# Optimization experiments

Measured on AMD Instinct MI355X. Metric: run time of the kernel, lower is better.

The kernel has to match this reference:

```python
import jax, jax.numpy as jnp
import numpy as np

EPS = 1e-5  # norm_eps


def setup_inputs() -> dict:
    key = jax.random.key(0)
    ks = jax.random.split(key, 9)
    N, C, T, H, W = 2, 1024, 8, 28, 28
    Di = 512
    s = 0.02  # weight init scale
    return {
        "x": jax.random.normal(ks[0], (N, C, T, H, W), jnp.float32),
        "w_theta": jax.random.normal(ks[1], (Di, C), jnp.float32) * s,
        "b_theta": jax.random.normal(ks[2], (Di,), jnp.float32) * s,
        "w_phi": jax.random.normal(ks[3], (Di, C), jnp.float32) * s,
        "b_phi": jax.random.normal(ks[4], (Di,), jnp.float32) * s,
        "w_g": jax.random.normal(ks[5], (Di, C), jnp.float32) * s,
        "b_g": jax.random.normal(ks[6], (Di,), jnp.float32) * s,
        "w_out": jax.random.normal(ks[7], (C, Di), jnp.float32) * s,
        "b_out": jax.random.normal(ks[8], (C,), jnp.float32) * s,
    }


def reference(x, w_theta, b_theta, w_phi, b_phi, w_g, b_g, w_out, b_out):
    # ProgressNL forward at step==0 (y == x), pool_size=None,
    # instantiation='softmax', norm_type='layernorm' (GroupNorm(1, C, affine=False)).
    N, C, T, H, W = x.shape
    Di = w_theta.shape[0]
    xf = x.reshape(N, C, T * H * W)  # flatten spatio-temporal tokens

    # 1x1x1 convs == per-token matmuls
    theta = jnp.einsum('dc,nct->ndt', w_theta, xf) + b_theta[None, :, None]  # [N,Di,THW]
    phi = jnp.einsum('dc,nct->ndt', w_phi, xf) + b_phi[None, :, None]
    g = jnp.einsum('dc,nct->ndt', w_g, xf) + b_g[None, :, None]

    # attention: softmax(theta^T phi / sqrt(Di)) @ g^T
    scores = jnp.einsum('nct,ncp->ntp', theta, phi) * (Di ** -0.5)  # [N,THW,THW]
    attn = jax.nn.softmax(scores, axis=-1)
    o = jnp.einsum('ntp,ncp->nct', attn, g)  # [N,Di,THW]

    # output 1x1x1 conv
    p = jnp.einsum('cd,ndt->nct', w_out, o) + b_out[None, :, None]  # [N,C,THW]

    # GroupNorm(1, C, affine=False): normalize over (C,T,H,W) per sample
    mean = jnp.mean(p, axis=(1, 2), keepdims=True)
    var = jnp.var(p, axis=(1, 2), keepdims=True)
    p = (p - mean) * jax.lax.rsqrt(var + EPS)

    return x + p.reshape(N, C, T, H, W)
```

## Files before the change

kernel.cpp:

```cpp
#include <hip/hip_runtime.h>

typedef _Float16 f16x8 __attribute__((ext_vector_type(8)));
typedef _Float16 f16x4 __attribute__((ext_vector_type(4)));
typedef float    f32x4 __attribute__((ext_vector_type(4)));

#define THW 6272
#define CCH 1024
#define DI  512

__device__ __forceinline__ void gload16(const _Float16* g, _Float16* l)
{
    __builtin_amdgcn_global_load_lds(
        (const __attribute__((address_space(1))) void*)g,
        (__attribute__((address_space(3))) void*)l, 16, 0, 0);
}

template<typename OUT_T, int BM, bool BIAS_M, bool BIAS_N, bool EXPP, bool GNP>
__global__ __launch_bounds__(256, 3)
void gemm_nt(const _Float16* __restrict__ A, size_t lda, size_t sAn,
             const _Float16* __restrict__ Bt, size_t ldb, size_t sBn,
             OUT_T* __restrict__ C, size_t ldc, size_t sCn,
             int K, float alpha,
             const float* __restrict__ bias_m,
             const float* __restrict__ bias_n,
             float* __restrict__ psum,
             int rows_ps,
             int gx, int gy)
{
    constexpr int MF = BM / 32;
    __shared__ _Float16 As[BM * 64];
    __shared__ _Float16 Bs[128 * 64];
    __shared__ float rs[4], rs2[4];
    const int tid  = threadIdx.x;
    const int lane = tid & 63;
    const int wave = tid >> 6;
    const int wr = wave >> 1, wc = wave & 1;

    const int nwg = gridDim.x;
    const int q = nwg >> 3, rr = nwg & 7;
    const int xcd = blockIdx.x & 7, seq = blockIdx.x >> 3;
    const int wg = (xcd < rr ? xcd * (q + 1) : rr * (q + 1) + (xcd - rr) * q) + seq;
    const int zz  = wg / (gx * gy);
    const int rem = wg - zz * gx * gy;
    const int by  = rem / gx, bx = rem - by * gx;
    const int n   = zz & 1;
    const int ks  = zz >> 1;

    A  += (size_t)n * sAn + (size_t)ks * K + (size_t)by * BM * lda;
    Bt += (size_t)n * sBn + (size_t)ks * K + (size_t)bx * 128 * ldb;

    const int srow = lane >> 3, sk = (lane & 7) * 8;
    const _Float16* gA = A  + (size_t)(wave * (MF * 8) + srow) * lda + sk;
    const _Float16* gB = Bt + (size_t)(wave * 32 + srow) * ldb + sk;
    _Float16* lA = As + wave * (MF * 512) + lane * 8;
    _Float16* lB = Bs + wave * 2048 + lane * 8;

    const int r  = lane & 15;
    const int kg = lane >> 4;

    f32x4 acc[MF][4] = {};

    for (int kt = 0; kt < K; kt += 64) {
#pragma unroll
        for (int i = 0; i < MF; i++)
            gload16(gA + (size_t)(i * 8) * lda, lA + i * 512);
#pragma unroll
        for (int i = 0; i < 4; i++)
            gload16(gB + (size_t)(i * 8) * ldb, lB + i * 512);
        gA += 64; gB += 64;
        __syncthreads();
#pragma unroll
        for (int kk = 0; kk < 2; kk++) {
            f16x8 af[MF], bf[4];
#pragma unroll
            for (int mf = 0; mf < MF; mf++)
                af[mf] = *(const f16x8*)(As + (wr * (BM / 2) + mf * 16 + r) * 64 + kk * 32 + kg * 8);
#pragma unroll
            for (int nf = 0; nf < 4; nf++)
                bf[nf] = *(const f16x8*)(Bs + (wc * 64 + nf * 16 + r) * 64 + kk * 32 + kg * 8);
#pragma unroll
            for (int mf = 0; mf < MF; mf++)
#pragma unroll
                for (int nf = 0; nf < 4; nf++)
                    acc[mf][nf] = __builtin_amdgcn_mfma_f32_16x16x32_f16(
                        af[mf], bf[nf], acc[mf][nf], 0, 0, 0);
        }
        __syncthreads();
    }

    C += (size_t)zz * sCn;
    float gs = 0.f, gs2 = 0.f;
#pragma unroll
    for (int mf = 0; mf < MF; mf++) {
#pragma unroll
        for (int qi = 0; qi < 4; qi++) {
            size_t row = (size_t)by * BM + wr * (BM / 2) + mf * 16 + kg * 4 + qi;
            float bm = BIAS_M ? bias_m[row] : 0.f;
            float rsum = 0.f;
#pragma unroll
            for (int nf = 0; nf < 4; nf++) {
                size_t col = (size_t)bx * 128 + wc * 64 + nf * 16 + r;
                float val = acc[mf][nf][qi] * alpha + bm + (BIAS_N ? bias_n[col] : 0.f);
                if (EXPP) {
                    float e = __expf(val);
                    rsum += e;
                    C[row * ldc + col] = (OUT_T)e;
                } else {
                    C[row * ldc + col] = (OUT_T)val;
                }
                if (GNP) { gs += val; gs2 += val * val; }
            }
            if (EXPP) {
                rsum += __shfl_xor(rsum, 1);
                rsum += __shfl_xor(rsum, 2);
                rsum += __shfl_xor(rsum, 4);
                rsum += __shfl_xor(rsum, 8);
                if (r == 0)
                    psum[((size_t)n * rows_ps + row) * 98 + bx * 2 + wc] = rsum;
            }
        }
    }
    if (GNP) {
        for (int o = 32; o; o >>= 1) {
            gs  += __shfl_xor(gs, o);
            gs2 += __shfl_xor(gs2, o);
        }
        if (lane == 0) { rs[wave] = gs; rs2[wave] = gs2; }
        __syncthreads();
        if (tid == 0) {
            psum[(size_t)wg * 2]     = rs[0] + rs[1] + rs[2] + rs[3];
            psum[(size_t)wg * 2 + 1] = rs2[0] + rs2[1] + rs2[2] + rs2[3];
        }
    }
}

__global__ __launch_bounds__(256)
void rowsum_inv(const float* __restrict__ psum, float* __restrict__ inv, int nrows)
{
    int rI = blockIdx.x * 256 + threadIdx.x;
    if (rI < nrows) {
        const float* p = psum + (size_t)rI * 98;
        float s = 0.f;
#pragma unroll 7
        for (int i = 0; i < 98; i++) s += p[i];
        inv[rI] = 1.f / s;
    }
}

__global__ __launch_bounds__(256)
void combine_scale(const float* __restrict__ Op, const float* __restrict__ inv,
                   _Float16* __restrict__ Ot, int tr, int t0)
{
    const int total4 = tr * 256;
    int idx = blockIdx.x * 256 + threadIdx.x;
    if (idx >= total4) return;
    const int per_n4 = tr * 128;
    int n = idx / per_n4;
    int rem = idx - n * per_n4;
    int t = rem >> 7, d4 = rem & 127;
    const f32x4* p = (const f32x4*)Op;
    f32x4 a = p[(size_t)n * per_n4 + rem];
    f32x4 b = p[(size_t)(2 + n) * per_n4 + rem];
    float sc = inv[(size_t)n * tr + t];
    f16x4 o;
#pragma unroll
    for (int j = 0; j < 4; j++) o[j] = (_Float16)((a[j] + b[j]) * sc);
    *(f16x4*)(Ot + ((size_t)(n * THW + t0 + t) * DI + d4 * 4)) = o;
}

__global__ __launch_bounds__(256)
void pack_weights(const float* __restrict__ wt, const float* __restrict__ wp,
                  const float* __restrict__ wg, const float* __restrict__ wo,
                  const float* __restrict__ bt, const float* __restrict__ bp,
                  _Float16* __restrict__ Wtp, _Float16* __restrict__ Wg,
                  _Float16* __restrict__ Wo, float* __restrict__ btp)
{
    int i = blockIdx.x * 256 + threadIdx.x;
    if (i < 512 * 1024) {
        Wtp[i]              = (_Float16)wt[i];
        Wtp[i + 512 * 1024] = (_Float16)wp[i];
        Wg[i]               = (_Float16)wg[i];
        Wo[i]               = (_Float16)wo[i];
    }
    if (i < 512) { btp[i] = bt[i]; btp[i + 512] = bp[i]; }
}

__global__ __launch_bounds__(256)
void transpose_cast(const float* __restrict__ x, _Float16* __restrict__ xT)
{
    __shared__ float tile[32][33];
    const int n  = blockIdx.z;
    const int t0 = blockIdx.x * 32;
    const int c0 = blockIdx.y * 32;
    const int tx = threadIdx.x & 31, ty = threadIdx.x >> 5;
    const float* xp = x + ((size_t)n * CCH + c0) * THW + t0;
#pragma unroll
    for (int i = 0; i < 4; i++) {
        int c = ty + i * 8;
        tile[c][tx] = xp[(size_t)c * THW + tx];
    }
    __syncthreads();
    _Float16* op = xT + ((size_t)n * THW + t0) * CCH + c0;
#pragma unroll
    for (int i = 0; i < 4; i++) {
        int t = ty + i * 8;
        op[(size_t)t * CCH + tx] = (_Float16)tile[tx][t];
    }
}

__global__ __launch_bounds__(256)
void reduce_final(const float* __restrict__ partials, float* __restrict__ stats, int nblk)
{
    const int n = blockIdx.x;
    float s = 0.f, s2 = 0.f;
    for (int i = threadIdx.x; i < nblk; i += 256) {
        s  += partials[((size_t)n * nblk + i) * 2];
        s2 += partials[((size_t)n * nblk + i) * 2 + 1];
    }
    for (int o = 32; o; o >>= 1) { s += __shfl_xor(s, o); s2 += __shfl_xor(s2, o); }
    __shared__ float rs[4], rs2[4];
    if ((threadIdx.x & 63) == 0) { rs[threadIdx.x >> 6] = s; rs2[threadIdx.x >> 6] = s2; }
    __syncthreads();
    if (threadIdx.x == 0) {
        float S1 = rs[0] + rs[1] + rs[2] + rs[3];
        float S2 = rs2[0] + rs2[1] + rs2[2] + rs2[3];
        const float invc = 1.f / ((float)CCH * (float)THW);
        float mean = S1 * invc;
        float var  = S2 * invc - mean * mean;
        stats[n * 2]     = mean;
        stats[n * 2 + 1] = rsqrtf(var + 1e-5f);
    }
}

__global__ __launch_bounds__(256)
void final_residual(const float* __restrict__ x, float* __restrict__ pc_out,
                    const float* __restrict__ stats, size_t total4)
{
    const size_t per_n4 = (size_t)CCH * THW / 4;
    for (size_t i = (size_t)blockIdx.x * 256 + threadIdx.x; i < total4;
         i += (size_t)gridDim.x * 256) {
        int n = (int)(i / per_n4);
        float mean = stats[n * 2], rstd = stats[n * 2 + 1];
        f32x4 xv = ((const f32x4*)x)[i];
        f32x4 pv = ((f32x4*)pc_out)[i];
        f32x4 ov;
#pragma unroll
        for (int j = 0; j < 4; j++) ov[j] = xv[j] + (pv[j] - mean) * rstd;
        ((f32x4*)pc_out)[i] = ov;
    }
}

extern "C" void kernel_launch(void* const* d_in, const int* in_sizes, int n_in,
                              void* d_out, int out_size, void* d_ws, size_t ws_size,
                              hipStream_t stream)
{
    const float* x  = (const float*)d_in[0];
    const float* wt = (const float*)d_in[1];
    const float* bt = (const float*)d_in[2];
    const float* wp = (const float*)d_in[3];
    const float* bp = (const float*)d_in[4];
    const float* wg = (const float*)d_in[5];
    const float* bg = (const float*)d_in[6];
    const float* wo = (const float*)d_in[7];
    const float* bo = (const float*)d_in[8];
    float* out = (float*)d_out;

    char* ws = (char*)d_ws;
    size_t off = 0;
    auto alloc = [&](size_t b) -> void* {
        off = (off + 255) & ~(size_t)255;
        void* p = ws + off;
        off += b;
        return p;
    };

    _Float16* Wtp = (_Float16*)alloc((size_t)1024 * 1024 * 2);
    _Float16* Wg  = (_Float16*)alloc((size_t)512 * 1024 * 2);
    _Float16* Wo  = (_Float16*)alloc((size_t)1024 * 512 * 2);
    float*    btp = (float*)alloc(1024 * 4);
    _Float16* xT  = (_Float16*)alloc((size_t)2 * THW * CCH * 2);
    _Float16* tpg = (_Float16*)alloc((size_t)2 * THW * 1024 * 2);
    _Float16* g   = (_Float16*)alloc((size_t)2 * DI * THW * 2);
    _Float16* Ot  = (_Float16*)alloc((size_t)2 * THW * DI * 2);
    float*    gnp   = (float*)alloc((size_t)784 * 2 * 4);
    float*    stats = (float*)alloc(4 * 4);

    const size_t tile_bytes = (size_t)2 * 128 * (THW * 2 + 98 * 4 + 4);
    size_t avail = (ws_size > off + 256) ? ws_size - off - 256 : 0;
    int tiles_fit = (int)(avail / tile_bytes);
    if (tiles_fit < 1) tiles_fit = 1;
    if (tiles_fit > 49) tiles_fit = 49;
    int nch = (49 + tiles_fit - 1) / tiles_fit;
    int tpc = (49 + nch - 1) / nch;

    _Float16* S    = (_Float16*)alloc((size_t)2 * tpc * 128 * THW * 2);
    float*    psum = (float*)alloc((size_t)2 * tpc * 128 * 98 * 4);
    float*    inv  = (float*)alloc((size_t)2 * tpc * 128 * 4);
    float*    Opart = out;

    const size_t sXT = (size_t)THW * CCH;
    const size_t sG  = (size_t)DI * THW;

    pack_weights<<<2048, 256, 0, stream>>>(wt, wp, wg, wo, bt, bp, Wtp, Wg, Wo, btp);
    transpose_cast<<<dim3(THW / 32, CCH / 32, 2), 256, 0, stream>>>(x, xT);

    gemm_nt<_Float16, 128, false, true, false, false><<<8 * 49 * 2, 256, 0, stream>>>(
        xT, CCH, sXT, Wtp, CCH, 0, tpg, 1024, sXT, CCH, 1.f,
        nullptr, btp, nullptr, 0, 8, 49);

    gemm_nt<_Float16, 64, true, false, false, false><<<49 * 8 * 2, 256, 0, stream>>>(
        Wg, CCH, 0, xT, CCH, sXT, g, THW, sG, CCH, 1.f,
        bg, nullptr, nullptr, 0, 49, 8);

    const float scale = 0.044194173824159216f;
    for (int ch = 0; ch < nch; ch++) {
        int tile0 = ch * tpc;
        int tiles = (49 - tile0 < tpc) ? (49 - tile0) : tpc;
        size_t t0 = (size_t)tile0 * 128;
        int tchRows = tiles * 128;

        gemm_nt<_Float16, 128, false, false, true, false><<<49 * tiles * 2, 256, 0, stream>>>(
            tpg + t0 * 1024, 1024, sXT, tpg + 512, 1024, sXT,
            S, THW, (size_t)tchRows * THW, DI, scale,
            nullptr, nullptr, psum, tchRows, 49, tiles);

        rowsum_inv<<<(2 * tchRows + 255) / 256, 256, 0, stream>>>(psum, inv, 2 * tchRows);

        gemm_nt<float, 128, false, false, false, false><<<4 * tiles * 4, 256, 0, stream>>>(
            S, THW, (size_t)tchRows * THW, g, THW, sG,
            Opart, DI, (size_t)tchRows * DI, THW / 2, 1.f,
            nullptr, nullptr, nullptr, 0, 4, tiles);

        combine_scale<<<(tchRows * 256 + 255) / 256, 256, 0, stream>>>(
            Opart, inv, Ot, tchRows, (int)t0);
    }

    gemm_nt<float, 128, true, false, false, true><<<49 * 8 * 2, 256, 0, stream>>>(
        Wo, DI, 0, Ot, DI, sG, out, THW, (size_t)CCH * THW, DI, 1.f,
        bo, nullptr, gnp, 0, 49, 8);

    reduce_final<<<2, 256, 0, stream>>>(gnp, stats, 392);
    final_residual<<<2048, 256, 0, stream>>>(x, out, stats, (size_t)2 * CCH * THW / 4);
}
```

Measured before the change: 452.3 us.

## Split attention PV GEMM four ways over K with fp16 partials and fused row scaling

The attention-times-g GEMM now splits its K dimension into four slices of 1600 instead of two halves, with a ragged last slice, which doubles the workgroup count for more parallelism. The softmax row normalization moves into the GEMM epilogue, and the partial outputs are stored as fp16 instead of fp32. The combine kernel becomes a 4-way fp16 sum. This targets low occupancy in the PV GEMM and the traffic of the partial buffers, at the cost of fp16 rounding on partial sums and an extra partial read in the combine step.

```diff
diff --git a/kernel.cpp b/kernel.cpp
--- a/kernel.cpp
+++ b/kernel.cpp
@@ -15,15 +15,16 @@
         (__attribute__((address_space(3))) void*)l, 16, 0, 0);
 }
 
-template<typename OUT_T, int BM, bool BIAS_M, bool BIAS_N, bool EXPP, bool GNP>
+template<typename OUT_T, int BM, bool BIAS_M, bool BIAS_N, bool EXPP, bool GNP, bool RSC>
 __global__ __launch_bounds__(256, 3)
 void gemm_nt(const _Float16* __restrict__ A, size_t lda, size_t sAn,
              const _Float16* __restrict__ Bt, size_t ldb, size_t sBn,
              OUT_T* __restrict__ C, size_t ldc, size_t sCn,
-             int K, float alpha,
+             int K, int Kfull, float alpha,
              const float* __restrict__ bias_m,
              const float* __restrict__ bias_n,
              float* __restrict__ psum,
+             const float* __restrict__ row_scale,
              int rows_ps,
              int gx, int gy)
 {
@@ -46,8 +47,11 @@
     const int n   = zz & 1;
     const int ks  = zz >> 1;
 
-    A  += (size_t)n * sAn + (size_t)ks * K + (size_t)by * BM * lda;
-    Bt += (size_t)n * sBn + (size_t)ks * K + (size_t)bx * 128 * ldb;
+    const int koff = ks * K;
+    const int klen = (Kfull - koff < K) ? (Kfull - koff) : K;
+
+    A  += (size_t)n * sAn + (size_t)by * BM * lda + koff;
+    Bt += (size_t)n * sBn + (size_t)bx * 128 * ldb + koff;
 
     const int srow = lane >> 3, sk = (lane & 7) * 8;
     const _Float16* gA = A  + (size_t)(wave * (MF * 8) + srow) * lda + sk;
@@ -60,7 +64,7 @@
 
     f32x4 acc[MF][4] = {};
 
-    for (int kt = 0; kt < K; kt += 64) {
+    for (int kt = 0; kt < klen; kt += 64) {
 #pragma unroll
         for (int i = 0; i < MF; i++)
             gload16(gA + (size_t)(i * 8) * lda, lA + i * 512);
@@ -96,6 +100,7 @@
         for (int qi = 0; qi < 4; qi++) {
             size_t row = (size_t)by * BM + wr * (BM / 2) + mf * 16 + kg * 4 + qi;
             float bm = BIAS_M ? bias_m[row] : 0.f;
+            float sc = RSC ? row_scale[(size_t)n * rows_ps + row] : 1.f;
             float rsum = 0.f;
 #pragma unroll
             for (int nf = 0; nf < 4; nf++) {
@@ -106,7 +111,7 @@
                     rsum += e;
                     C[row * ldc + col] = (OUT_T)e;
                 } else {
-                    C[row * ldc + col] = (OUT_T)val;
+                    C[row * ldc + col] = (OUT_T)(RSC ? val * sc : val);
                 }
                 if (GNP) { gs += val; gs2 += val * val; }
             }
@@ -148,24 +153,27 @@
 }
 
 __global__ __launch_bounds__(256)
-void combine_scale(const float* __restrict__ Op, const float* __restrict__ inv,
-                   _Float16* __restrict__ Ot, int tr, int t0)
-{
-    const int total4 = tr * 256;
+void combine4(const _Float16* __restrict__ Op, _Float16* __restrict__ Ot,
+              int tr, int t0)
+{
+    const int per_n8 = tr * 64;
     int idx = blockIdx.x * 256 + threadIdx.x;
-    if (idx >= total4) return;
-    const int per_n4 = tr * 128;
-    int n = idx / per_n4;
-    int rem = idx - n * per_n4;
-    int t = rem >> 7, d4 = rem & 127;
-    const f32x4* p = (const f32x4*)Op;
-    f32x4 a = p[(size_t)n * per_n4 + rem];
-    f32x4 b = p[(size_t)(2 + n) * per_n4 + rem];
-    float sc = inv[(size_t)n * tr + t];
-    f16x4 o;
-#pragma unroll
-    for (int j = 0; j < 4; j++) o[j] = (_Float16)((a[j] + b[j]) * sc);
-    *(f16x4*)(Ot + ((size_t)(n * THW + t0 + t) * DI + d4 * 4)) = o;
+    if (idx >= 2 * per_n8) return;
+    int n = idx / per_n8;
+    int rem = idx - n * per_n8;
+    int t = rem >> 6, d8 = rem & 63;
+    const size_t slice = (size_t)tr * 512;
+    float o[8] = {};
+#pragma unroll
+    for (int ks = 0; ks < 4; ks++) {
+        f16x8 v = *(const f16x8*)(Op + (size_t)(ks * 2 + n) * slice + (size_t)rem * 8);
+#pragma unroll
+        for (int j = 0; j < 8; j++) o[j] += (float)v[j];
+    }
+    f16x8 w;
+#pragma unroll
+    for (int j = 0; j < 8; j++) w[j] = (_Float16)o[j];
+    *(f16x8*)(Ot + ((size_t)(n * THW + t0 + t) * DI + d8 * 8)) = w;
 }
 
 __global__ __launch_bounds__(256)
@@ -296,7 +304,7 @@
     _Float16* S    = (_Float16*)alloc((size_t)2 * tpc * 128 * THW * 2);
     float*    psum = (float*)alloc((size_t)2 * tpc * 128 * 98 * 4);
     float*    inv  = (float*)alloc((size_t)2 * tpc * 128 * 4);
-    float*    Opart = out;
+    _Float16* Opart = (_Float16*)out;
 
     const size_t sXT = (size_t)THW * CCH;
     const size_t sG  = (size_t)DI * THW;
@@ -304,13 +312,13 @@
     pack_weights<<<2048, 256, 0, stream>>>(wt, wp, wg, wo, bt, bp, Wtp, Wg, Wo, btp);
     transpose_cast<<<dim3(THW / 32, CCH / 32, 2), 256, 0, stream>>>(x, xT);
 
-    gemm_nt<_Float16, 128, false, true, false, false><<<8 * 49 * 2, 256, 0, stream>>>(
-        xT, CCH, sXT, Wtp, CCH, 0, tpg, 1024, sXT, CCH, 1.f,
-        nullptr, btp, nullptr, 0, 8, 49);
-
-    gemm_nt<_Float16, 64, true, false, false, false><<<49 * 8 * 2, 256, 0, stream>>>(
-        Wg, CCH, 0, xT, CCH, sXT, g, THW, sG, CCH, 1.f,
-        bg, nullptr, nullptr, 0, 49, 8);
+    gemm_nt<_Float16, 128, false, true, false, false, false><<<8 * 49 * 2, 256, 0, stream>>>(
+        xT, CCH, sXT, Wtp, CCH, 0, tpg, 1024, sXT, CCH, CCH, 1.f,
+        nullptr, btp, nullptr, nullptr, 0, 8, 49);
+
+    gemm_nt<_Float16, 64, true, false, false, false, false><<<49 * 8 * 2, 256, 0, stream>>>(
+        Wg, CCH, 0, xT, CCH, sXT, g, THW, sG, CCH, CCH, 1.f,
+        bg, nullptr, nullptr, nullptr, 0, 49, 8);
 
     const float scale = 0.044194173824159216f;
     for (int ch = 0; ch < nch; ch++) {
@@ -319,25 +327,25 @@
         size_t t0 = (size_t)tile0 * 128;
         int tchRows = tiles * 128;
 
-        gemm_nt<_Float16, 128, false, false, true, false><<<49 * tiles * 2, 256, 0, stream>>>(
+        gemm_nt<_Float16, 128, false, false, true, false, false><<<49 * tiles * 2, 256, 0, stream>>>(
             tpg + t0 * 1024, 1024, sXT, tpg + 512, 1024, sXT,
-            S, THW, (size_t)tchRows * THW, DI, scale,
-            nullptr, nullptr, psum, tchRows, 49, tiles);
+            S, THW, (size_t)tchRows * THW, DI, DI, scale,
+            nullptr, nullptr, psum, nullptr, tchRows, 49, tiles);
 
         rowsum_inv<<<(2 * tchRows + 255) / 256, 256, 0, stream>>>(psum, inv, 2 * tchRows);
 
-        gemm_nt<float, 128, false, false, false, false><<<4 * tiles * 4, 256, 0, stream>>>(
+        gemm_nt<_Float16, 128, false, false, false, false, true><<<4 * tiles * 8, 256, 0, stream>>>(
             S, THW, (size_t)tchRows * THW, g, THW, sG,
-            Opart, DI, (size_t)tchRows * DI, THW / 2, 1.f,
-            nullptr, nullptr, nullptr, 0, 4, tiles);
-
-        combine_scale<<<(tchRows * 256 + 255) / 256, 256, 0, stream>>>(
-            Opart, inv, Ot, tchRows, (int)t0);
-    }
-
-    gemm_nt<float, 128, true, false, false, true><<<49 * 8 * 2, 256, 0, stream>>>(
-        Wo, DI, 0, Ot, DI, sG, out, THW, (size_t)CCH * THW, DI, 1.f,
-        bo, nullptr, gnp, 0, 49, 8);
+            Opart, DI, (size_t)tchRows * DI, 1600, THW, 1.f,
+            nullptr, nullptr, nullptr, inv, tchRows, 4, tiles);
+
+        combine4<<<(tchRows * 128 + 255) / 256, 256, 0, stream>>>(
+            Opart, Ot, tchRows, (int)t0);
+    }
+
+    gemm_nt<float, 128, true, false, false, true, false><<<49 * 8 * 2, 256, 0, stream>>>(
+        Wo, DI, 0, Ot, DI, sG, out, THW, (size_t)CCH * THW, DI, DI, 1.f,
+        bo, nullptr, gnp, nullptr, 0, 49, 8);
 
     reduce_final<<<2, 256, 0, stream>>>(gnp, stats, 392);
     final_residual<<<2048, 256, 0, stream>>>(x, out, stats, (size_t)2 * CCH * THW / 4);
```

After: 395.2 us. 1.14x faster.
